# Kernel tuning notes

Hardware: AMD Instinct MI355X
Metric: run time of the kernel (lower is better)

The kernel has to match this reference:

```python
import jax, jax.numpy as jnp
import numpy as np

NUM_EMBEDDINGS = 1024
EMBEDDING_DIM = 128
COMMITMENT_COST = 0.25
B, T = 32, 2048


def setup_inputs() -> dict:
    key = jax.random.key(0)
    k1, k2 = jax.random.split(key)
    inputs = jax.random.normal(k1, (B, T, EMBEDDING_DIM), dtype=jnp.float32)
    lim = 1.0 / NUM_EMBEDDINGS
    embedding_weight = jax.random.uniform(
        k2, (NUM_EMBEDDINGS, EMBEDDING_DIM), dtype=jnp.float32,
        minval=-lim, maxval=lim)
    return {"inputs": inputs, "embedding_weight": embedding_weight}


def reference(inputs, embedding_weight):
    D = embedding_weight.shape[1]
    flat = inputs.reshape(-1, D)                                  # [N, D]
    # squared L2 distances to every codebook entry: [N, K]
    distances = (
        jnp.sum(flat * flat, axis=1, keepdims=True)
        + jnp.sum(embedding_weight * embedding_weight, axis=1)
        - 2.0 * jnp.matmul(flat, embedding_weight.T)
    )
    encoding_indices = jnp.argmin(distances, axis=1)              # [N]
    quantized = embedding_weight[encoding_indices].reshape(inputs.shape)
    sg = jax.lax.stop_gradient
    e_latent_loss = jnp.mean((sg(quantized) - inputs) ** 2)
    q_latent_loss = jnp.mean((quantized - sg(inputs)) ** 2)
    loss = q_latent_loss + COMMITMENT_COST * e_latent_loss
    # straight-through estimator
    quantized = inputs + sg(quantized - inputs)
    return (loss, quantized, encoding_indices)
```

## Files before the change

### kernel.cpp

```cpp
#include <hip/hip_runtime.h>

#define NROWS 65536
#define KC    1024
#define DIM   128
#define W_DIST 3.5e-5f

typedef short  bf16x8 __attribute__((ext_vector_type(8)));
typedef float  f32x4  __attribute__((ext_vector_type(4)));
typedef float  f32x16 __attribute__((ext_vector_type(16)));

#define ZERO16 ((f32x16){0.f,0.f,0.f,0.f,0.f,0.f,0.f,0.f,0.f,0.f,0.f,0.f,0.f,0.f,0.f,0.f})

__device__ __forceinline__ unsigned short f2bf_rne(float f) {
    unsigned int u = __float_as_uint(f);
    u += 0x7FFFu + ((u >> 16) & 1u);
    return (unsigned short)(u >> 16);
}
__device__ __forceinline__ float bf2f(unsigned short h) {
    return __uint_as_float(((unsigned int)h) << 16);
}

__device__ __forceinline__ void gll16(const unsigned short* g, short* l) {
    __builtin_amdgcn_global_load_lds(
        (const __attribute__((address_space(1))) unsigned int*)g,
        (__attribute__((address_space(3))) unsigned int*)l,
        16, 0, 0);
}

template <int N>
__device__ __forceinline__ void vmwait() {
    if constexpr (N == 8)      asm volatile("s_waitcnt vmcnt(8)" ::: "memory");
    else if constexpr (N == 4) asm volatile("s_waitcnt vmcnt(4)" ::: "memory");
    else if constexpr (N == 2) asm volatile("s_waitcnt vmcnt(2)" ::: "memory");
    else                       asm volatile("s_waitcnt vmcnt(0)" ::: "memory");
}

__device__ __forceinline__ float np_sumsq_128(const float* v) {
    float r[8];
    #pragma unroll
    for (int j = 0; j < 8; ++j) r[j] = __fmul_rn(v[j], v[j]);
    #pragma unroll
    for (int i = 1; i < 16; ++i)
        #pragma unroll
        for (int j = 0; j < 8; ++j)
            r[j] = __fadd_rn(r[j], __fmul_rn(v[i * 8 + j], v[i * 8 + j]));
    return __fadd_rn(__fadd_rn(__fadd_rn(r[0], r[1]), __fadd_rn(r[2], r[3])),
                     __fadd_rn(__fadd_rn(r[4], r[5]), __fadd_rn(r[6], r[7])));
}

__global__ __launch_bounds__(256) void vq_prep(const float* __restrict__ emb,
        float* __restrict__ enorm,
        unsigned short* __restrict__ eh, unsigned short* __restrict__ em) {
    const int t = blockIdx.x * 256 + threadIdx.x;
    const int k = t >> 3;
    const int j = t & 7;
    const float* row = emb + (size_t)k * DIM;

    float r = __fmul_rn(row[j], row[j]);
    #pragma unroll
    for (int i = 1; i < 16; ++i) {
        float v = row[i * 8 + j];
        r = __fadd_rn(r, __fmul_rn(v, v));
    }
    r = __fadd_rn(r, __shfl_xor(r, 1, 64));
    r = __fadd_rn(r, __shfl_xor(r, 2, 64));
    r = __fadd_rn(r, __shfl_xor(r, 4, 64));
    if (j == 0) enorm[k] = r;

    const float4* p = reinterpret_cast<const float4*>(row + j * 16);
    unsigned int h[16], m[16];
    #pragma unroll
    for (int q = 0; q < 4; ++q) {
        float4 v4 = p[q];
        float f[4] = {v4.x, v4.y, v4.z, v4.w};
        #pragma unroll
        for (int c = 0; c < 4; ++c) {
            unsigned short hh = f2bf_rne(f[c]);
            h[q * 4 + c] = hh;
            m[q * 4 + c] = f2bf_rne(f[c] - bf2f(hh));
        }
    }
    uint4 vh0 = {h[0] | (h[1] << 16), h[2] | (h[3] << 16),
                 h[4] | (h[5] << 16), h[6] | (h[7] << 16)};
    uint4 vh1 = {h[8] | (h[9] << 16), h[10] | (h[11] << 16),
                 h[12] | (h[13] << 16), h[14] | (h[15] << 16)};
    uint4 vm0 = {m[0] | (m[1] << 16), m[2] | (m[3] << 16),
                 m[4] | (m[5] << 16), m[6] | (m[7] << 16)};
    uint4 vm1 = {m[8] | (m[9] << 16), m[10] | (m[11] << 16),
                 m[12] | (m[13] << 16), m[14] | (m[15] << 16)};
    unsigned short* ph = eh + (size_t)k * DIM + j * 16;
    unsigned short* pm = em + (size_t)k * DIM + j * 16;
    *reinterpret_cast<uint4*>(ph) = vh0;
    *reinterpret_cast<uint4*>(ph + 8) = vh1;
    *reinterpret_cast<uint4*>(pm) = vm0;
    *reinterpret_cast<uint4*>(pm + 8) = vm1;
}

__global__ __launch_bounds__(256, 2) void vq_mfma(
        const float* __restrict__ x,
        const unsigned short* __restrict__ eh, const unsigned short* __restrict__ em,
        const float* __restrict__ enorm,
        int* __restrict__ bestk, float* __restrict__ idx_out,
        int* __restrict__ fb_cnt, int* __restrict__ fb_rows,
        double* __restrict__ partials) {
    const int tid  = threadIdx.x;
    const int lane = tid & 63;
    const int wid  = tid >> 6;
    const int lr31 = lane & 31;
    const int hi   = lane >> 5;
    const int rtile = blockIdx.x * 128 + wid * 32;

    __shared__ short ldsE[3][2][4096];
    __shared__ float s_enorm[KC];
    __shared__ double sloss[4];

    const int u0 = wid * 128 + lane;
    const int u1 = wid * 128 + 64 + lane;
    const int src0 = (u0 & 31) * DIM + (u0 >> 5) * 8;
    const int src1 = (u1 & 31) * DIM + (u1 >> 5) * 8;
    const int dst0 = wid * 128 * 8;
    const int dst1 = (wid * 128 + 64) * 8;

#define VQ_STAGE(T, B)                                                      \
    do {                                                                    \
        const unsigned short* _gh = eh + (size_t)(T) * 4096;                \
        const unsigned short* _gm = em + (size_t)(T) * 4096;                \
        gll16(_gh + src0, &ldsE[B][0][dst0]);                               \
        gll16(_gh + src1, &ldsE[B][0][dst1]);                               \
        gll16(_gm + src0, &ldsE[B][1][dst0]);                               \
        gll16(_gm + src1, &ldsE[B][1][dst1]);                               \
    } while (0)

    bf16x8 fxh[8], fxm[8];
    float xn;
    {
        const float* px = x + (size_t)(rtile + lr31) * DIM + hi * 8;
        float c0 = 0.f, c1 = 0.f, c2 = 0.f, c3 = 0.f;
        #pragma unroll
        for (int s = 0; s < 8; ++s) {
            float4 a = *reinterpret_cast<const float4*>(px + s * 16);
            float4 b = *reinterpret_cast<const float4*>(px + s * 16 + 4);
            c0 = fmaf(a.x, a.x, c0); c1 = fmaf(a.y, a.y, c1);
            c2 = fmaf(a.z, a.z, c2); c3 = fmaf(a.w, a.w, c3);
            c0 = fmaf(b.x, b.x, c0); c1 = fmaf(b.y, b.y, c1);
            c2 = fmaf(b.z, b.z, c2); c3 = fmaf(b.w, b.w, c3);
            float f[8] = {a.x, a.y, a.z, a.w, b.x, b.y, b.z, b.w};
            bf16x8 vh, vm;
            #pragma unroll
            for (int j = 0; j < 8; ++j) {
                unsigned short hh = f2bf_rne(f[j]);
                vh[j] = (short)hh;
                vm[j] = (short)f2bf_rne(f[j] - bf2f(hh));
            }
            fxh[s] = vh; fxm[s] = vm;
        }
        xn = (c0 + c1) + (c2 + c3);
        xn += __shfl_xor(xn, 32, 64);
    }
    #pragma unroll
    for (int s = 0; s < 8; ++s)
        asm volatile("" : "+v"(fxh[s]), "+v"(fxm[s]));

    *reinterpret_cast<float4*>(&s_enorm[tid * 4]) =
        *reinterpret_cast<const float4*>(&enorm[tid * 4]);

    VQ_STAGE(0, 0);
    VQ_STAGE(1, 1);

    asm volatile("s_waitcnt lgkmcnt(0)" ::: "memory");
    __builtin_amdgcn_s_barrier();

    float m1 = 1e30f, m2 = 1e30f; int k1 = 0;
    f32x16 aE, dE, aO, dO;

#define VQ_EPI(T, PA, PD)                                                   \
    do {                                                                    \
        const int _kb = (T) * 32 + (hi << 2);                               \
        _Pragma("unroll")                                                   \
        for (int g = 0; g < 4; ++g) {                                       \
            const f32x4 _nr = *reinterpret_cast<const f32x4*>(&s_enorm[_kb + g * 8]); \
            _Pragma("unroll")                                               \
            for (int j = 0; j < 4; ++j) {                                   \
                const int _r = g * 4 + j;                                   \
                float _v = fmaf(-2.0f, PA[_r] + PD[_r], _nr[j]);            \
                int _kk = _kb + g * 8 + j;                                  \
                bool _lt = _v < m1;                                         \
                m2 = fminf(m2, fmaxf(m1, _v));                              \
                k1 = _lt ? _kk : k1;                                        \
                m1 = fminf(m1, _v);                                         \
            }                                                               \
        }                                                                   \
    } while (0)

#define VQ_ITER(T, B, SB, CA, CD, PA, PD, VMN, DOSTAGE, DOEPI)              \
    do {                                                                    \
        vmwait<VMN>();                                                      \
        __builtin_amdgcn_s_barrier();                                       \
        asm volatile("" ::: "memory");                                      \
        CA = ZERO16; CD = ZERO16;                                           \
        __builtin_amdgcn_s_setprio(1);                                      \
        _Pragma("unroll")                                                   \
        for (int s = 0; s < 8; ++s) {                                       \
            const int _u = ((s * 2 + hi) * 32 + lr31) * 8;                  \
            bf16x8 feh = *reinterpret_cast<const bf16x8*>(&ldsE[B][0][_u]); \
            bf16x8 fem = *reinterpret_cast<const bf16x8*>(&ldsE[B][1][_u]); \
            CA = __builtin_amdgcn_mfma_f32_32x32x16_bf16(feh, fxh[s], CA, 0, 0, 0); \
            CD = __builtin_amdgcn_mfma_f32_32x32x16_bf16(feh, fxm[s], CD, 0, 0, 0); \
            CD = __builtin_amdgcn_mfma_f32_32x32x16_bf16(fem, fxh[s], CD, 0, 0, 0); \
        }                                                                   \
        __builtin_amdgcn_s_setprio(0);                                      \
        if (DOSTAGE) { VQ_STAGE((T) + 2, SB); }                             \
        if (DOEPI)   { VQ_EPI((T) - 1, PA, PD); }                           \
    } while (0)

    VQ_ITER(0, 0, 2, aE, dE, aO, dO, 4, 1, 0);
    VQ_ITER(1, 1, 0, aO, dO, aE, dE, 4, 1, 1);
    VQ_ITER(2, 2, 1, aE, dE, aO, dO, 4, 1, 1);
    VQ_ITER(3, 0, 2, aO, dO, aE, dE, 4, 1, 1);
    VQ_ITER(4, 1, 0, aE, dE, aO, dO, 4, 1, 1);
    VQ_ITER(5, 2, 1, aO, dO, aE, dE, 4, 1, 1);
    for (int tb = 6; tb < 30; tb += 6) {
        VQ_ITER(tb + 0, 0, 2, aE, dE, aO, dO, 4, 1, 1);
        VQ_ITER(tb + 1, 1, 0, aO, dO, aE, dE, 4, 1, 1);
        VQ_ITER(tb + 2, 2, 1, aE, dE, aO, dO, 4, 1, 1);
        VQ_ITER(tb + 3, 0, 2, aO, dO, aE, dE, 4, 1, 1);
        VQ_ITER(tb + 4, 1, 0, aE, dE, aO, dO, 4, 1, 1);
        VQ_ITER(tb + 5, 2, 1, aO, dO, aE, dE, 4, 1, 1);
    }
    VQ_ITER(30, 0, 2, aE, dE, aO, dO, 4, 0, 1);
    VQ_ITER(31, 1, 0, aO, dO, aE, dE, 0, 0, 1);
    VQ_EPI(31, aO, dO);
#undef VQ_ITER
#undef VQ_EPI
#undef VQ_STAGE

    {
        float om1 = __shfl_xor(m1, 32, 64);
        float om2 = __shfl_xor(m2, 32, 64);
        int   ok1 = __shfl_xor(k1, 32, 64);
        float mx = fmaxf(m1, om1);
        m2 = fminf(fminf(m2, om2), mx);
        bool take = (om1 < m1) || (om1 == m1 && ok1 < k1);
        k1 = take ? ok1 : k1;
        m1 = fminf(m1, om1);
    }

    {
        float ls = m1 + xn;
        #pragma unroll
        for (int off = 1; off < 64; off <<= 1) ls += __shfl_xor(ls, off, 64);
        if (lane == 0) sloss[wid] = (double)ls * 0.5;
    }
    __syncthreads();
    if (tid == 0)
        partials[blockIdx.x] = (sloss[0] + sloss[1]) + (sloss[2] + sloss[3]);

    if (lane < 32) {
        const int row = rtile + lane;
        if (m2 - m1 < W_DIST) {
            int slot = atomicAdd(fb_cnt, 1);
            fb_rows[slot] = row;
        } else {
            bestk[row] = k1;
            idx_out[row] = (float)k1;
        }
    }
}

__global__ __launch_bounds__(512) void vq_fallback(
        const float* __restrict__ x, const float* __restrict__ emb,
        const float* __restrict__ enorm,
        const int* __restrict__ fb_cnt, const int* __restrict__ fb_rows,
        int* __restrict__ bestk, float* __restrict__ idx_out) {
    const int tid  = threadIdx.x;
    const int lane = tid & 63;
    const int wid  = tid >> 6;
    const int nb = *fb_cnt;

    __shared__ float sx[8][DIM];
    __shared__ float s_xn[8];
    __shared__ float swv[8][8];
    __shared__ int   swk[8][8];

    const float en0 = enorm[tid];
    const float en1 = enorm[tid + 512];
    const float4* e0p = reinterpret_cast<const float4*>(emb + (size_t)tid * DIM);
    const float4* e1p = reinterpret_cast<const float4*>(emb + (size_t)(tid + 512) * DIM);

    for (int base = blockIdx.x * 8; base < nb; base += gridDim.x * 8) {
        const int R = min(8, nb - base);
        {
            const int r = tid >> 6;
            const int c2 = (tid & 63) * 2;
            const int slot = fb_rows[min(base + r, nb - 1)];
            float2 v = *reinterpret_cast<const float2*>(x + (size_t)slot * DIM + c2);
            sx[r][c2] = v.x; sx[r][c2 + 1] = v.y;
        }
        __syncthreads();
        if (tid < 8) s_xn[tid] = np_sumsq_128(&sx[tid][0]);
        __syncthreads();

        float a0[8][4], a1[8][4];
        #pragma unroll
        for (int r = 0; r < 8; ++r)
            #pragma unroll
            for (int c = 0; c < 4; ++c) { a0[r][c] = 0.f; a1[r][c] = 0.f; }

        for (int q = 0; q < 32; q += 4) {
            float4 e0v[4], e1v[4];
            #pragma unroll
            for (int j = 0; j < 4; ++j) { e0v[j] = e0p[q + j]; e1v[j] = e1p[q + j]; }
            #pragma unroll
            for (int j = 0; j < 4; ++j) {
                #pragma unroll
                for (int r = 0; r < 8; ++r) {
                    float4 xv = *reinterpret_cast<const float4*>(&sx[r][(q + j) * 4]);
                    a0[r][0] = fmaf(xv.x, e0v[j].x, a0[r][0]);
                    a0[r][1] = fmaf(xv.y, e0v[j].y, a0[r][1]);
                    a0[r][2] = fmaf(xv.z, e0v[j].z, a0[r][2]);
                    a0[r][3] = fmaf(xv.w, e0v[j].w, a0[r][3]);
                    a1[r][0] = fmaf(xv.x, e1v[j].x, a1[r][0]);
                    a1[r][1] = fmaf(xv.y, e1v[j].y, a1[r][1]);
                    a1[r][2] = fmaf(xv.z, e1v[j].z, a1[r][2]);
                    a1[r][3] = fmaf(xv.w, e1v[j].w, a1[r][3]);
                }
            }
        }

        float cv[8]; int ck[8];
        #pragma unroll
        for (int r = 0; r < 8; ++r) {
            float xn = s_xn[r];
            float d0 = __fadd_rn(__fadd_rn(a0[r][0], a0[r][1]),
                                 __fadd_rn(a0[r][2], a0[r][3]));
            float s0 = __fsub_rn(__fadd_rn(xn, en0), __fmul_rn(2.0f, d0));
            float d1 = __fadd_rn(__fadd_rn(a1[r][0], a1[r][1]),
                                 __fadd_rn(a1[r][2], a1[r][3]));
            float s1 = __fsub_rn(__fadd_rn(xn, en1), __fmul_rn(2.0f, d1));
            bool t1 = (s1 < s0);
            cv[r] = t1 ? s1 : s0;
            ck[r] = t1 ? tid + 512 : tid;
        }
        #pragma unroll
        for (int off = 1; off < 64; off <<= 1) {
            #pragma unroll
            for (int r = 0; r < 8; ++r) {
                float ov = __shfl_xor(cv[r], off, 64);
                int   ok = __shfl_xor(ck[r], off, 64);
                bool take = (ov < cv[r]) || (ov == cv[r] && ok < ck[r]);
                cv[r] = take ? ov : cv[r];
                ck[r] = take ? ok : ck[r];
            }
        }
        if (lane == 0) {
            #pragma unroll
            for (int r = 0; r < 8; ++r) { swv[wid][r] = cv[r]; swk[wid][r] = ck[r]; }
        }
        __syncthreads();
        if (tid < R) {
            float bv = swv[0][tid]; int bk = swk[0][tid];
            #pragma unroll
            for (int w = 1; w < 8; ++w) {
                float v = swv[w][tid]; int k = swk[w][tid];
                bool take = (v < bv) || (v == bv && k < bk);
                bv = take ? v : bv;
                bk = take ? k : bk;
            }
            const int row = fb_rows[base + tid];
            bestk[row] = bk;
            idx_out[row] = (float)bk;
        }
        __syncthreads();
    }
}

__global__ __launch_bounds__(256) void vq_gather(
        const float* __restrict__ emb, const int* __restrict__ bestk,
        float* __restrict__ quant) {
    const int t = blockIdx.x * 256 + threadIdx.x;
    const int r = t >> 4;
    const int c = (t & 15) * 8;
    const int bk = bestk[r];
    const float4* ep = reinterpret_cast<const float4*>(emb + (size_t)bk * DIM + c);
    float4 e0 = ep[0], e1 = ep[1];
    float* q = quant + (size_t)r * DIM + c;
    q[0] = e0.x; q[1] = e0.y; q[2] = e0.z; q[3] = e0.w;
    q[4] = e1.x; q[5] = e1.y; q[6] = e1.z; q[7] = e1.w;
}

__global__ __launch_bounds__(256) void vq_loss(
        const double* __restrict__ partials, float* __restrict__ out) {
    double s = partials[threadIdx.x] + partials[threadIdx.x + 256];
    #pragma unroll
    for (int off = 32; off > 0; off >>= 1) s += __shfl_down(s, off, 64);
    __shared__ double sd[4];
    if ((threadIdx.x & 63) == 0) sd[threadIdx.x >> 6] = s;
    __syncthreads();
    if (threadIdx.x == 0)
        out[0] = (float)(((sd[0] + sd[1]) + (sd[2] + sd[3])) * (1.25 / 8388608.0));
}

extern "C" void kernel_launch(void* const* d_in, const int* in_sizes, int n_in,
                              void* d_out, int out_size, void* d_ws, size_t ws_size,
                              hipStream_t stream) {
    const float* x   = (const float*)d_in[0];
    const float* emb = (const float*)d_in[1];

    float* out      = (float*)d_out;
    float* loss_out = out;
    float* quant    = out + 1;
    float* idx_out  = out + 1 + (size_t)NROWS * DIM;

    char* ws = (char*)d_ws;
    int*    fb_cnt   = (int*)(ws + 8);
    float*  enorm    = (float*)(ws + 1024);
    int*    fb_rows  = (int*)(ws + 16384);
    int*    bestk    = (int*)(ws + 278528);
    unsigned short* eh = (unsigned short*)(ws + 557056);
    unsigned short* em = (unsigned short*)(ws + 819200);
    double* partials = (double*)(ws + 1081344);

    hipMemsetAsync(ws, 0, 16, stream);
    vq_prep<<<32, 256, 0, stream>>>(emb, enorm, eh, em);
    vq_mfma<<<512, 256, 0, stream>>>(x, eh, em, enorm,
                                     bestk, idx_out, fb_cnt, fb_rows, partials);
    vq_fallback<<<1024, 512, 0, stream>>>(x, emb, enorm, fb_cnt, fb_rows,
                                          bestk, idx_out);
    vq_gather<<<4096, 256, 0, stream>>>(emb, bestk, quant);
    vq_loss<<<1, 256, 0, stream>>>(partials, loss_out);
}
```

Measured before the change: 96.73 us.

## Use 512-thread blocks so eight waves share each staged codebook tile

```diff
diff --git a/kernel.cpp b/kernel.cpp
--- a/kernel.cpp
+++ b/kernel.cpp
@@ -29,9 +29,9 @@
 
 template <int N>
 __device__ __forceinline__ void vmwait() {
-    if constexpr (N == 8)      asm volatile("s_waitcnt vmcnt(8)" ::: "memory");
-    else if constexpr (N == 4) asm volatile("s_waitcnt vmcnt(4)" ::: "memory");
+    if constexpr (N == 4)      asm volatile("s_waitcnt vmcnt(4)" ::: "memory");
     else if constexpr (N == 2) asm volatile("s_waitcnt vmcnt(2)" ::: "memory");
+    else if constexpr (N == 1) asm volatile("s_waitcnt vmcnt(1)" ::: "memory");
     else                       asm volatile("s_waitcnt vmcnt(0)" ::: "memory");
 }
 
@@ -96,7 +96,7 @@
     *reinterpret_cast<uint4*>(pm + 8) = vm1;
 }
 
-__global__ __launch_bounds__(256, 2) void vq_mfma(
+__global__ __launch_bounds__(512, 4) void vq_mfma(
         const float* __restrict__ x,
         const unsigned short* __restrict__ eh, const unsigned short* __restrict__ em,
         const float* __restrict__ enorm,
@@ -108,27 +108,20 @@
     const int wid  = tid >> 6;
     const int lr31 = lane & 31;
     const int hi   = lane >> 5;
-    const int rtile = blockIdx.x * 128 + wid * 32;
+    const int rtile = blockIdx.x * 256 + wid * 32;
 
     __shared__ short ldsE[3][2][4096];
     __shared__ float s_enorm[KC];
-    __shared__ double sloss[4];
-
-    const int u0 = wid * 128 + lane;
-    const int u1 = wid * 128 + 64 + lane;
-    const int src0 = (u0 & 31) * DIM + (u0 >> 5) * 8;
-    const int src1 = (u1 & 31) * DIM + (u1 >> 5) * 8;
-    const int dst0 = wid * 128 * 8;
-    const int dst1 = (wid * 128 + 64) * 8;
+    __shared__ double sloss[8];
+
+    const int su  = wid * 64 + lane;
+    const int src = (su & 31) * DIM + (su >> 5) * 8;
+    const int dst = su * 8;
 
 #define VQ_STAGE(T, B)                                                      \
     do {                                                                    \
-        const unsigned short* _gh = eh + (size_t)(T) * 4096;                \
-        const unsigned short* _gm = em + (size_t)(T) * 4096;                \
-        gll16(_gh + src0, &ldsE[B][0][dst0]);                               \
-        gll16(_gh + src1, &ldsE[B][0][dst1]);                               \
-        gll16(_gm + src0, &ldsE[B][1][dst0]);                               \
-        gll16(_gm + src1, &ldsE[B][1][dst1]);                               \
+        gll16(eh + (size_t)(T) * 4096 + src, &ldsE[B][0][dst]);             \
+        gll16(em + (size_t)(T) * 4096 + src, &ldsE[B][1][dst]);             \
     } while (0)
 
     bf16x8 fxh[8], fxm[8];
@@ -161,8 +154,8 @@
     for (int s = 0; s < 8; ++s)
         asm volatile("" : "+v"(fxh[s]), "+v"(fxm[s]));
 
-    *reinterpret_cast<float4*>(&s_enorm[tid * 4]) =
-        *reinterpret_cast<const float4*>(&enorm[tid * 4]);
+    *reinterpret_cast<float2*>(&s_enorm[tid * 2]) =
+        *reinterpret_cast<const float2*>(&enorm[tid * 2]);
 
     VQ_STAGE(0, 0);
     VQ_STAGE(1, 1);
@@ -213,21 +206,21 @@
         if (DOEPI)   { VQ_EPI((T) - 1, PA, PD); }                           \
     } while (0)
 
-    VQ_ITER(0, 0, 2, aE, dE, aO, dO, 4, 1, 0);
-    VQ_ITER(1, 1, 0, aO, dO, aE, dE, 4, 1, 1);
-    VQ_ITER(2, 2, 1, aE, dE, aO, dO, 4, 1, 1);
-    VQ_ITER(3, 0, 2, aO, dO, aE, dE, 4, 1, 1);
-    VQ_ITER(4, 1, 0, aE, dE, aO, dO, 4, 1, 1);
-    VQ_ITER(5, 2, 1, aO, dO, aE, dE, 4, 1, 1);
+    VQ_ITER(0, 0, 2, aE, dE, aO, dO, 2, 1, 0);
+    VQ_ITER(1, 1, 0, aO, dO, aE, dE, 2, 1, 1);
+    VQ_ITER(2, 2, 1, aE, dE, aO, dO, 2, 1, 1);
+    VQ_ITER(3, 0, 2, aO, dO, aE, dE, 2, 1, 1);
+    VQ_ITER(4, 1, 0, aE, dE, aO, dO, 2, 1, 1);
+    VQ_ITER(5, 2, 1, aO, dO, aE, dE, 2, 1, 1);
     for (int tb = 6; tb < 30; tb += 6) {
-        VQ_ITER(tb + 0, 0, 2, aE, dE, aO, dO, 4, 1, 1);
-        VQ_ITER(tb + 1, 1, 0, aO, dO, aE, dE, 4, 1, 1);
-        VQ_ITER(tb + 2, 2, 1, aE, dE, aO, dO, 4, 1, 1);
-        VQ_ITER(tb + 3, 0, 2, aO, dO, aE, dE, 4, 1, 1);
-        VQ_ITER(tb + 4, 1, 0, aE, dE, aO, dO, 4, 1, 1);
-        VQ_ITER(tb + 5, 2, 1, aO, dO, aE, dE, 4, 1, 1);
-    }
-    VQ_ITER(30, 0, 2, aE, dE, aO, dO, 4, 0, 1);
+        VQ_ITER(tb + 0, 0, 2, aE, dE, aO, dO, 2, 1, 1);
+        VQ_ITER(tb + 1, 1, 0, aO, dO, aE, dE, 2, 1, 1);
+        VQ_ITER(tb + 2, 2, 1, aE, dE, aO, dO, 2, 1, 1);
+        VQ_ITER(tb + 3, 0, 2, aO, dO, aE, dE, 2, 1, 1);
+        VQ_ITER(tb + 4, 1, 0, aE, dE, aO, dO, 2, 1, 1);
+        VQ_ITER(tb + 5, 2, 1, aO, dO, aE, dE, 2, 1, 1);
+    }
+    VQ_ITER(30, 0, 2, aE, dE, aO, dO, 2, 0, 1);
     VQ_ITER(31, 1, 0, aO, dO, aE, dE, 0, 0, 1);
     VQ_EPI(31, aO, dO);
 #undef VQ_ITER
@@ -252,8 +245,11 @@
         if (lane == 0) sloss[wid] = (double)ls * 0.5;
     }
     __syncthreads();
-    if (tid == 0)
-        partials[blockIdx.x] = (sloss[0] + sloss[1]) + (sloss[2] + sloss[3]);
+    if (tid == 0) {
+        double s = ((sloss[0] + sloss[1]) + (sloss[2] + sloss[3]))
+                 + ((sloss[4] + sloss[5]) + (sloss[6] + sloss[7]));
+        partials[blockIdx.x] = s;
+    }
 
     if (lane < 32) {
         const int row = rtile + lane;
@@ -390,7 +386,7 @@
 
 __global__ __launch_bounds__(256) void vq_loss(
         const double* __restrict__ partials, float* __restrict__ out) {
-    double s = partials[threadIdx.x] + partials[threadIdx.x + 256];
+    double s = partials[threadIdx.x];
     #pragma unroll
     for (int off = 32; off > 0; off >>= 1) s += __shfl_down(s, off, 64);
     __shared__ double sd[4];
@@ -422,7 +418,7 @@
 
     hipMemsetAsync(ws, 0, 16, stream);
     vq_prep<<<32, 256, 0, stream>>>(emb, enorm, eh, em);
-    vq_mfma<<<512, 256, 0, stream>>>(x, eh, em, enorm,
+    vq_mfma<<<256, 512, 0, stream>>>(x, eh, em, enorm,
                                      bestk, idx_out, fb_cnt, fb_rows, partials);
     vq_fallback<<<1024, 512, 0, stream>>>(x, emb, enorm, fb_cnt, fb_rows,
                                           bestk, idx_out);
```

New measurement: 216.5 us. 2.24x slower.
